# Optimization experiments

Measured on AMD Instinct MI355X. Metric: run time of the kernel, lower is better.

The kernel has to match this reference:

```python
import jax, jax.numpy as jnp
import numpy as np

B, T, V, E, H, D = 32, 64, 32000, 512, 1024, 1024
BOS, EOS, PAD, TAU = 1, 3, 0, 1.0


def setup_inputs() -> dict:
    key = jax.random.key(0)
    ks = jax.random.split(key, 8)
    s = lambda k, shape, sc=0.02: jax.random.normal(k, shape, jnp.float32) * sc
    return {
        'image_hidden': jax.random.normal(ks[0], (B, D), jnp.float32),
        'gumbel_u': jax.random.uniform(ks[1], (T, B, V), jnp.float32),
        'W_proj': s(ks[2], (H, D)), 'b_proj': jnp.zeros((H,), jnp.float32),
        'emb': s(ks[3], (V, E)),
        'W_ih': s(ks[4], (4 * H, E)), 'W_hh': s(ks[5], (4 * H, H)),
        'b_ih': jnp.zeros((4 * H,), jnp.float32), 'b_hh': jnp.zeros((4 * H,), jnp.float32),
        'W_hv': s(ks[6], (V, H)), 'b_hv': jnp.zeros((V,), jnp.float32),
    }


def lstm_cell(x, h, c, W_ih, W_hh, b_ih, b_hh):
    gates = x @ W_ih.T + h @ W_hh.T + (b_ih + b_hh)
    i, f, g, o = jnp.split(gates, 4, axis=-1)  # torch LSTM gate order
    c = jax.nn.sigmoid(f) * c + jax.nn.sigmoid(i) * jnp.tanh(g)
    h = jax.nn.sigmoid(o) * jnp.tanh(c)
    return h, c


def reference(image_hidden, gumbel_u, W_proj, b_proj, emb, W_ih, W_hh, b_ih, b_hh, W_hv, b_hv):
    # initial state from projected image representation
    h0 = image_hidden @ W_proj.T + b_proj            # [B, H]
    c0 = jnp.zeros_like(h0)
    x0 = jnp.broadcast_to(emb[BOS], (B, E))          # BOS embedding
    h, c = lstm_cell(x0, h0, c0, W_ih, W_hh, b_ih, b_hh)

    def step(carry, u):
        h, c = carry
        logit = h @ W_hv.T + b_hv                    # [B, V]
        g = -jnp.log(-jnp.log(u + 1e-10) + 1e-10)    # gumbel noise from uniform
        y_soft = jax.nn.softmax((logit + g) / TAU, axis=-1)
        label = jnp.argmax(y_soft, axis=-1)          # [B]
        y_hard = jax.nn.one_hot(label, V, dtype=y_soft.dtype)
        y = y_hard + y_soft - jax.lax.stop_gradient(y_soft)  # straight-through (hard=True)
        x = y @ emb                                  # soft embedding lookup [B, E]
        h, c = lstm_cell(x, h, c, W_ih, W_hh, b_ih, b_hh)
        return (h, c), (y, label)

    _, (ys, labels) = jax.lax.scan(step, (h, c), gumbel_u)
    logits = jnp.swapaxes(ys, 0, 1)                  # [B, T, V]
    labels = labels.T                                # [B, T]

    # force final token to EOS
    logits = logits.at[:, -1, :].set(jax.nn.one_hot(EOS, V, dtype=logits.dtype))
    labels = labels.at[:, -1].set(EOS)

    pad_g = jnp.cumsum((labels == EOS).astype(jnp.int32), axis=1) == 0  # True before first EOS
    message_ids = jnp.where(pad_g, labels, 0)
    pad_oh = jax.nn.one_hot(PAD, V, dtype=logits.dtype)
    message_logits = jnp.where(pad_g[:, :, None], logits, pad_oh)
    message_lengths = jnp.max(jnp.cumsum(pad_g.astype(jnp.int32), axis=1), axis=1) + 1
    return message_ids, message_logits, message_lengths
```

## Files before the change

kernel.cpp:

```cpp
#include <hip/hip_runtime.h>
#include <cstdint>
#include <cstddef>

#define NB 32
#define NT 64
#define NV 32000
#define NE 512
#define NH 1024
#define BOS_ID 1
#define EOS_ID 3

__device__ __forceinline__ unsigned mono_f32(float f) {
    unsigned u = __float_as_uint(f);
    return (u & 0x80000000u) ? ~u : (u | 0x80000000u);
}

__global__ __launch_bounds__(256) void k_init(const float* __restrict__ img,
                                              const float* __restrict__ Wp,
                                              const float* __restrict__ bp,
                                              float* __restrict__ h0,
                                              float* __restrict__ c) {
    int g = blockIdx.x * 256 + threadIdx.x;
    int j = g >> 5, b = g & 31;
    const float* ir = img + (size_t)b * NH;
    const float* wr = Wp + (size_t)j * NH;
    float s = bp[j];
    for (int k = 0; k < NH; k++) s = fmaf(ir[k], wr[k], s);
    h0[b * NH + j] = s;
    c[b * NH + j]  = 0.0f;
}

__global__ __launch_bounds__(512) void k_logit(const float* __restrict__ h,
                                               const float* __restrict__ Whv,
                                               const float* __restrict__ bhv,
                                               const float* __restrict__ gu,
                                               int s,
                                               unsigned long long* __restrict__ slot) {
    __shared__ __align__(16) float Wlds[64][64];
    const int tid = threadIdx.x;
    const int l   = tid & 63;
    const int w   = tid >> 6;
    const int v   = blockIdx.x * 64 + l;
    const int lm  = l & 7;

    const int vv  = tid >> 3;
    const int kq2 = tid & 7;
    const float* __restrict__ wsrc =
        Whv + (size_t)(blockIdx.x * 64 + vv) * NH + kq2 * 8;
    const int q0 = (2 * kq2 + 0) ^ (vv & 7);
    const int q1 = (2 * kq2 + 1) ^ (vv & 7);

    const float* __restrict__ h0p = h + (w * 4 + 0) * NH;
    const float* __restrict__ h1p = h + (w * 4 + 1) * NH;
    const float* __restrict__ h2p = h + (w * 4 + 2) * NH;
    const float* __restrict__ h3p = h + (w * 4 + 3) * NH;

    float acc[4];
#pragma unroll
    for (int bi = 0; bi < 4; bi++) acc[bi] = 0.f;

    float4 st0, st1;
    st0 = *(const float4*)(wsrc + 0);
    st1 = *(const float4*)(wsrc + 4);

    for (int c = 0; c < 16; c++) {
        __syncthreads();
        *(float4*)&Wlds[vv][q0 * 4] = st0;
        *(float4*)&Wlds[vv][q1 * 4] = st1;
        if (c < 15) {
            st0 = *(const float4*)(wsrc + (c + 1) * 64);
            st1 = *(const float4*)(wsrc + (c + 1) * 64 + 4);
        }
        __syncthreads();

        const int kc = c * 64;
        float4 hc0 = *(const float4*)&h0p[kc];
        float4 hc1 = *(const float4*)&h1p[kc];
        float4 hc2 = *(const float4*)&h2p[kc];
        float4 hc3 = *(const float4*)&h3p[kc];
#pragma unroll
        for (int t = 0; t < 16; t++) {
            float4 hn0, hn1, hn2, hn3;
            if (t < 15) {
                const int kn = kc + 4 * (t + 1);
                hn0 = *(const float4*)&h0p[kn];
                hn1 = *(const float4*)&h1p[kn];
                hn2 = *(const float4*)&h2p[kn];
                hn3 = *(const float4*)&h3p[kn];
            }
            const float4 w4 = *(const float4*)&Wlds[l][4 * (t ^ lm)];
            acc[0] = fmaf(hc0.x, w4.x, acc[0]); acc[0] = fmaf(hc0.y, w4.y, acc[0]);
            acc[0] = fmaf(hc0.z, w4.z, acc[0]); acc[0] = fmaf(hc0.w, w4.w, acc[0]);
            acc[1] = fmaf(hc1.x, w4.x, acc[1]); acc[1] = fmaf(hc1.y, w4.y, acc[1]);
            acc[1] = fmaf(hc1.z, w4.z, acc[1]); acc[1] = fmaf(hc1.w, w4.w, acc[1]);
            acc[2] = fmaf(hc2.x, w4.x, acc[2]); acc[2] = fmaf(hc2.y, w4.y, acc[2]);
            acc[2] = fmaf(hc2.z, w4.z, acc[2]); acc[2] = fmaf(hc2.w, w4.w, acc[2]);
            acc[3] = fmaf(hc3.x, w4.x, acc[3]); acc[3] = fmaf(hc3.y, w4.y, acc[3]);
            acc[3] = fmaf(hc3.z, w4.z, acc[3]); acc[3] = fmaf(hc3.w, w4.w, acc[3]);
            if (t < 15) { hc0 = hn0; hc1 = hn1; hc2 = hn2; hc3 = hn3; }
        }
    }

    const float bv = bhv[v];
    const size_t gubase = (size_t)s * NB * NV;
#pragma unroll
    for (int bi = 0; bi < 4; bi++) {
        const int b = w * 4 + bi;
        float u  = gu[gubase + (size_t)b * NV + v];
        float g  = -logf(-logf(u + 1e-10f) + 1e-10f);
        float sc = acc[bi] + bv + g;
        unsigned long long key =
            ((unsigned long long)mono_f32(sc) << 32) | (unsigned)(~(unsigned)v);
#pragma unroll
        for (int m = 1; m < 64; m <<= 1) {
            unsigned long long o =
                (unsigned long long)__shfl_xor((long long)key, m, 64);
            if (o > key) key = o;
        }
        if (l == 0) atomicMax(&slot[(s & 1) * 32 + b], key);
    }
}

__global__ __launch_bounds__(256) void k_lstm(const float* __restrict__ h,
                                              float* __restrict__ hn,
                                              float* __restrict__ cbuf,
                                              const float* __restrict__ emb,
                                              const float* __restrict__ Wih,
                                              const float* __restrict__ Whh,
                                              const float* __restrict__ bih,
                                              const float* __restrict__ bhh,
                                              unsigned long long* __restrict__ slot,
                                              int* __restrict__ hist,
                                              int s, int skip) {
    __shared__ float Wt[512][20];
    __shared__ float xh[32][517];
    __shared__ int labels[32];
    const int tid = threadIdx.x, blk = blockIdx.x;
    const int b8 = tid >> 3, ks = tid & 7;

    if (s < 0) {
        if (tid < 32) labels[tid] = BOS_ID;
    } else {
        if (tid < 32) labels[tid] = (int)(~(unsigned)slot[(s & 1) * 32 + tid]);
    }
    if (tid >= 32 && tid < 64)
        slot[((s + 1) & 1) * 32 + (tid - 32)] = 0ull;
    if (s >= 0 && blk == 0 && tid < 32) hist[s * 32 + tid] = labels[tid];
    if (skip) return;

    const int j0 = blk * 4;
    float acc[16];
#pragma unroll
    for (int r = 0; r < 16; r++) acc[r] = 0.f;

    float wreg[32];
    float xreg[64];
    auto issue = [&](int chunk) {
#pragma unroll
        for (int i = 0; i < 32; i++) {
            int idx = i * 256 + tid;
            int slot_i = idx >> 9, k = idx & 511;
            int gate = slot_i >> 2, jj = slot_i & 3;
            int row = gate * NH + j0 + jj;
            wreg[i] = (chunk == 0) ? Wih[(size_t)row * NE + k]
                                   : Whh[(size_t)row * NH + (chunk - 1) * 512 + k];
        }
#pragma unroll
        for (int i = 0; i < 64; i++) {
            int idx = i * 256 + tid;
            int b = idx >> 9, k = idx & 511;
            xreg[i] = (chunk == 0) ? emb[(size_t)labels[b] * NE + k]
                                   : h[b * NH + (chunk - 1) * 512 + k];
        }
    };

    __syncthreads();
    issue(0);
    for (int chunk = 0; chunk < 3; chunk++) {
        __syncthreads();
#pragma unroll
        for (int i = 0; i < 32; i++) {
            int idx = i * 256 + tid;
            Wt[idx & 511][idx >> 9] = wreg[i];
        }
#pragma unroll
        for (int i = 0; i < 64; i++) {
            int idx = i * 256 + tid;
            xh[idx >> 9][idx & 511] = xreg[i];
        }
        if (chunk < 2) issue(chunk + 1);
        __syncthreads();
#pragma unroll 4
        for (int i = 0; i < 64; i++) {
            int k = ks + 8 * i;
            float xv = xh[b8][k];
            const float4 w0 = *(const float4*)&Wt[k][0];
            const float4 w1 = *(const float4*)&Wt[k][4];
            const float4 w2 = *(const float4*)&Wt[k][8];
            const float4 w3 = *(const float4*)&Wt[k][12];
            acc[0]  = fmaf(xv, w0.x, acc[0]);  acc[1]  = fmaf(xv, w0.y, acc[1]);
            acc[2]  = fmaf(xv, w0.z, acc[2]);  acc[3]  = fmaf(xv, w0.w, acc[3]);
            acc[4]  = fmaf(xv, w1.x, acc[4]);  acc[5]  = fmaf(xv, w1.y, acc[5]);
            acc[6]  = fmaf(xv, w1.z, acc[6]);  acc[7]  = fmaf(xv, w1.w, acc[7]);
            acc[8]  = fmaf(xv, w2.x, acc[8]);  acc[9]  = fmaf(xv, w2.y, acc[9]);
            acc[10] = fmaf(xv, w2.z, acc[10]); acc[11] = fmaf(xv, w2.w, acc[11]);
            acc[12] = fmaf(xv, w3.x, acc[12]); acc[13] = fmaf(xv, w3.y, acc[13]);
            acc[14] = fmaf(xv, w3.z, acc[14]); acc[15] = fmaf(xv, w3.w, acc[15]);
        }
    }
#pragma unroll
    for (int m = 1; m < 8; m <<= 1)
#pragma unroll
        for (int r = 0; r < 16; r++) acc[r] += __shfl_xor(acc[r], m, 64);

    if (ks == 0) {
        int b = b8;
#pragma unroll
        for (int jj = 0; jj < 4; jj++) {
            int j = j0 + jj;
            float gi = acc[0 + jj]  + bih[j]          + bhh[j];
            float gf = acc[4 + jj]  + bih[NH + j]     + bhh[NH + j];
            float gg = acc[8 + jj]  + bih[2 * NH + j] + bhh[2 * NH + j];
            float go = acc[12 + jj] + bih[3 * NH + j] + bhh[3 * NH + j];
            float si = 1.f / (1.f + expf(-gi));
            float sf = 1.f / (1.f + expf(-gf));
            float so = 1.f / (1.f + expf(-go));
            float cn = sf * cbuf[b * NH + j] + si * tanhf(gg);
            float hv = so * tanhf(cn);
            cbuf[b * NH + j] = cn;
            hn[b * NH + j]   = hv;
        }
    }
}

__global__ __launch_bounds__(64) void k_out(const int* __restrict__ hist,
                                            float* __restrict__ out) {
    int b = threadIdx.x;
    if (b >= 32) return;
    int te = 63;
    for (int t = 0; t < 63; t++)
        if (hist[t * 32 + b] == EOS_ID) { te = t; break; }
    for (int t = 0; t < 64; t++) {
        int lab = (t < 63) ? hist[t * 32 + b] : EOS_ID;
        int id = (t < te) ? lab : 0;
        out[b * 64 + t] = (float)id;
    }
    out[2048 + (size_t)NB * NT * NV + b] = (float)(te + 1);
}

__global__ __launch_bounds__(256) void k_scatter(float* __restrict__ out) {
    const int bt = blockIdx.x;
    float* row = out + 2048 + (size_t)bt * NV;
    const int id = (int)out[bt];
    float4 z = make_float4(0.f, 0.f, 0.f, 0.f);
    for (int i = threadIdx.x; i < NV / 4; i += 256) ((float4*)row)[i] = z;
    __syncthreads();
    if (threadIdx.x == 0) row[id] = 1.0f;
}

extern "C" void kernel_launch(void* const* d_in, const int* in_sizes, int n_in,
                              void* d_out, int out_size, void* d_ws, size_t ws_size,
                              hipStream_t stream) {
    const float* img = (const float*)d_in[0];
    const float* gu  = (const float*)d_in[1];
    const float* Wp  = (const float*)d_in[2];
    const float* bp  = (const float*)d_in[3];
    const float* emb = (const float*)d_in[4];
    const float* Wih = (const float*)d_in[5];
    const float* Whh = (const float*)d_in[6];
    const float* bih = (const float*)d_in[7];
    const float* bhh = (const float*)d_in[8];
    const float* Whv = (const float*)d_in[9];
    const float* bhv = (const float*)d_in[10];
    float* out = (float*)d_out;

    float* scratch = out + 2048;
    float* hA = scratch;
    float* hB = scratch + 32768;
    float* cb = scratch + 65536;
    unsigned long long* slot = (unsigned long long*)(scratch + 98304);
    int* hist = (int*)(scratch + 98304 + 128);

    k_init<<<128, 256, 0, stream>>>(img, Wp, bp, hB, cb);
    k_lstm<<<256, 256, 0, stream>>>(hB, hA, cb, emb, Wih, Whh, bih, bhh,
                                    slot, hist, -1, 0);
    for (int s = 0; s < 63; s++) {
        const float* hc = (s & 1) ? hB : hA;
        float* hn       = (s & 1) ? hA : hB;
        k_logit<<<500, 512, 0, stream>>>(hc, Whv, bhv, gu, s, slot);
        k_lstm<<<256, 256, 0, stream>>>(hc, hn, cb, emb, Wih, Whh, bih, bhh,
                                        slot, hist, s, (s == 62) ? 1 : 0);
    }
    k_out<<<1, 64, 0, stream>>>(hist, out);
    k_scatter<<<2048, 256, 0, stream>>>(out);
}
```

Before: 13.81 ms.

## Split K across half-waves in logit kernel and double grid size

Each k_logit block now covers 32 vocabulary rows instead of 64. The two halves of each wavefront work on separate halves of the hidden dimension and combine their partial sums with a cross-lane shuffle. The grid doubles to 1000 blocks, which should spread the W_hv streaming more evenly across compute units and cut tail imbalance. The register-level prefetch of h is dropped in favour of direct loads, and the epilogue now repeats the gumbel and argmax work in both half-waves.

New measurement: 16.89 ms. 1.22x slower.

```diff
diff --git a/kernel.cpp b/kernel.cpp
--- a/kernel.cpp
+++ b/kernel.cpp
@@ -36,69 +36,72 @@
                                                const float* __restrict__ gu,
                                                int s,
                                                unsigned long long* __restrict__ slot) {
-    __shared__ __align__(16) float Wlds[64][64];
+    __shared__ __align__(16) float Wlds[32][128];
     const int tid = threadIdx.x;
     const int l   = tid & 63;
     const int w   = tid >> 6;
-    const int v   = blockIdx.x * 64 + l;
-    const int lm  = l & 7;
-
-    const int vv  = tid >> 3;
-    const int kq2 = tid & 7;
+    const int lo  = l & 31;
+    const int h2  = l >> 5;
+    const int v   = blockIdx.x * 32 + lo;
+    const int lm  = lo & 7;
+
+    const int r   = tid >> 4;
+    const int hs  = (tid >> 3) & 1;
+    const int i8  = tid & 7;
     const float* __restrict__ wsrc =
-        Whv + (size_t)(blockIdx.x * 64 + vv) * NH + kq2 * 8;
-    const int q0 = (2 * kq2 + 0) ^ (vv & 7);
-    const int q1 = (2 * kq2 + 1) ^ (vv & 7);
-
-    const float* __restrict__ h0p = h + (w * 4 + 0) * NH;
-    const float* __restrict__ h1p = h + (w * 4 + 1) * NH;
-    const float* __restrict__ h2p = h + (w * 4 + 2) * NH;
-    const float* __restrict__ h3p = h + (w * 4 + 3) * NH;
+        Whv + (size_t)(blockIdx.x * 32 + r) * NH + hs * 512 + i8 * 8;
+    float* const dst0 = &Wlds[r][hs * 64 + (((2 * i8 + 0) ^ (r & 7)) << 2)];
+    float* const dst1 = &Wlds[r][hs * 64 + (((2 * i8 + 1) ^ (r & 7)) << 2)];
+
+    const float* __restrict__ hb0 = h + (w * 4 + 0) * NH + h2 * 512;
+    const float* __restrict__ hb1 = h + (w * 4 + 1) * NH + h2 * 512;
+    const float* __restrict__ hb2 = h + (w * 4 + 2) * NH + h2 * 512;
+    const float* __restrict__ hb3 = h + (w * 4 + 3) * NH + h2 * 512;
 
     float acc[4];
 #pragma unroll
     for (int bi = 0; bi < 4; bi++) acc[bi] = 0.f;
 
-    float4 st0, st1;
-    st0 = *(const float4*)(wsrc + 0);
-    st1 = *(const float4*)(wsrc + 4);
-
-    for (int c = 0; c < 16; c++) {
-        __syncthreads();
-        *(float4*)&Wlds[vv][q0 * 4] = st0;
-        *(float4*)&Wlds[vv][q1 * 4] = st1;
-        if (c < 15) {
+    float4 st0 = *(const float4*)(wsrc + 0);
+    float4 st1 = *(const float4*)(wsrc + 4);
+
+    for (int c = 0; c < 8; c++) {
+        __syncthreads();
+        *(float4*)dst0 = st0;
+        *(float4*)dst1 = st1;
+        if (c < 7) {
             st0 = *(const float4*)(wsrc + (c + 1) * 64);
             st1 = *(const float4*)(wsrc + (c + 1) * 64 + 4);
         }
         __syncthreads();
 
         const int kc = c * 64;
-        float4 hc0 = *(const float4*)&h0p[kc];
-        float4 hc1 = *(const float4*)&h1p[kc];
-        float4 hc2 = *(const float4*)&h2p[kc];
-        float4 hc3 = *(const float4*)&h3p[kc];
+        const float* __restrict__ p0 = hb0 + kc;
+        const float* __restrict__ p1 = hb1 + kc;
+        const float* __restrict__ p2 = hb2 + kc;
+        const float* __restrict__ p3 = hb3 + kc;
 #pragma unroll
         for (int t = 0; t < 16; t++) {
-            float4 hn0, hn1, hn2, hn3;
-            if (t < 15) {
-                const int kn = kc + 4 * (t + 1);
-                hn0 = *(const float4*)&h0p[kn];
-                hn1 = *(const float4*)&h1p[kn];
-                hn2 = *(const float4*)&h2p[kn];
-                hn3 = *(const float4*)&h3p[kn];
-            }
-            const float4 w4 = *(const float4*)&Wlds[l][4 * (t ^ lm)];
-            acc[0] = fmaf(hc0.x, w4.x, acc[0]); acc[0] = fmaf(hc0.y, w4.y, acc[0]);
-            acc[0] = fmaf(hc0.z, w4.z, acc[0]); acc[0] = fmaf(hc0.w, w4.w, acc[0]);
-            acc[1] = fmaf(hc1.x, w4.x, acc[1]); acc[1] = fmaf(hc1.y, w4.y, acc[1]);
-            acc[1] = fmaf(hc1.z, w4.z, acc[1]); acc[1] = fmaf(hc1.w, w4.w, acc[1]);
-            acc[2] = fmaf(hc2.x, w4.x, acc[2]); acc[2] = fmaf(hc2.y, w4.y, acc[2]);
-            acc[2] = fmaf(hc2.z, w4.z, acc[2]); acc[2] = fmaf(hc2.w, w4.w, acc[2]);
-            acc[3] = fmaf(hc3.x, w4.x, acc[3]); acc[3] = fmaf(hc3.y, w4.y, acc[3]);
-            acc[3] = fmaf(hc3.z, w4.z, acc[3]); acc[3] = fmaf(hc3.w, w4.w, acc[3]);
-            if (t < 15) { hc0 = hn0; hc1 = hn1; hc2 = hn2; hc3 = hn3; }
-        }
+            const float4 w4 = *(const float4*)&Wlds[lo][h2 * 64 + ((t ^ lm) << 2)];
+            const float4 ha = *(const float4*)&p0[4 * t];
+            const float4 hb = *(const float4*)&p1[4 * t];
+            const float4 hc = *(const float4*)&p2[4 * t];
+            const float4 hd = *(const float4*)&p3[4 * t];
+            acc[0] = fmaf(ha.x, w4.x, acc[0]); acc[0] = fmaf(ha.y, w4.y, acc[0]);
+            acc[0] = fmaf(ha.z, w4.z, acc[0]); acc[0] = fmaf(ha.w, w4.w, acc[0]);
+            acc[1] = fmaf(hb.x, w4.x, acc[1]); acc[1] = fmaf(hb.y, w4.y, acc[1]);
+            acc[1] = fmaf(hb.z, w4.z, acc[1]); acc[1] = fmaf(hb.w, w4.w, acc[1]);
+            acc[2] = fmaf(hc.x, w4.x, acc[2]); acc[2] = fmaf(hc.y, w4.y, acc[2]);
+            acc[2] = fmaf(hc.z, w4.z, acc[2]); acc[2] = fmaf(hc.w, w4.w, acc[2]);
+            acc[3] = fmaf(hd.x, w4.x, acc[3]); acc[3] = fmaf(hd.y, w4.y, acc[3]);
+            acc[3] = fmaf(hd.z, w4.z, acc[3]); acc[3] = fmaf(hd.w, w4.w, acc[3]);
+        }
+    }
+
+#pragma unroll
+    for (int bi = 0; bi < 4; bi++) {
+        float o = __shfl_xor(acc[bi], 32, 64);
+        acc[bi] = (h2 == 0) ? (acc[bi] + o) : (o + acc[bi]);
     }
 
     const float bv = bhv[v];
@@ -287,7 +290,7 @@
     for (int s = 0; s < 63; s++) {
         const float* hc = (s & 1) ? hB : hA;
         float* hn       = (s & 1) ? hA : hB;
-        k_logit<<<500, 512, 0, stream>>>(hc, Whv, bhv, gu, s, slot);
+        k_logit<<<1000, 512, 0, stream>>>(hc, Whv, bhv, gu, s, slot);
         k_lstm<<<256, 256, 0, stream>>>(hc, hn, cb, emb, Wih, Whh, bih, bhh,
                                         slot, hist, s, (s == 62) ? 1 : 0);
     }
```
